# Performance work log

Hardware: AMD Instinct MI355X
Metric: run time of the kernel (lower is better)

## Reference

```python
import jax, jax.numpy as jnp
import numpy as np

B, TQ, TKV, NPR, H, D = 4, 1024, 1024, 5, 16, 64
IN, OUT, R, P, NT = 1024, H * D, 64, 4096, 4
KV = NPR + TKV  # prompt tokens prepended to kv sequence


def setup_inputs() -> dict:
    key = jax.random.key(0)
    ks = jax.random.split(key, 20)
    n = lambda k, shp, s: jax.random.normal(k, shp, jnp.float32) * s
    W = 0.02  # weight init scale
    return {
        "pe": n(ks[0], (P, OUT), 1.0),
        "attn_output": n(ks[1], (B, TQ, OUT), 1.0),
        "q": n(ks[2], (B, H, TQ, D), 1.0),
        "kv_query": n(ks[3], (B, TKV, IN), 1.0),
        "attn_mask": jnp.zeros((TQ, KV), jnp.float32),
        "prompt": n(ks[4], (NT, NPR, IN), 1.0),
        "gates": n(ks[5], (1,), 1.0),
        "k_w1": n(ks[6], (IN, R), W), "k_w2": n(ks[7], (R, OUT), W),
        "v_w1": n(ks[8], (IN, R), W), "v_w2": n(ks[9], (R, OUT), W),
        "kp_w1": n(ks[10], (OUT, R), W), "kp_w2": n(ks[11], (R, OUT), W),
        "qp_w1": n(ks[12], (OUT, R), W), "qp_w2": n(ks[13], (R, OUT), W),
        "indices_a": jax.random.randint(ks[14], (B, TQ), 0, P),
        "indices_b": jax.random.randint(ks[15], (B, TKV), 0, P),
        "task_idx": jax.random.randint(ks[16], (B,), 0, NT),
    }


def reference(pe, attn_output, q, kv_query, attn_mask, prompt, gates,
              k_w1, k_w2, v_w1, v_w2, kp_w1, kp_w2, qp_w1, qp_w2,
              indices_a, indices_b, task_idx):
    # prompt selection + concat in front of kv sequence
    pr = prompt[task_idx]                                   # [B, NPR, IN]
    kv_x = jnp.concatenate([pr, kv_query], axis=1)          # [B, KV, IN]
    # positional features; key_pos is zero-padded over the prompt slots
    key_pos = jnp.pad(pe[indices_b], ((0, 0), (NPR, 0), (0, 0)))  # [B, KV, OUT]
    # low-rank projections
    k = (kv_x @ k_w1) @ k_w2 + (key_pos @ kp_w1) @ kp_w2    # [B, KV, OUT]
    v = (kv_x @ v_w1) @ v_w2                                # [B, KV, OUT]
    q_pos = (pe[indices_a] @ qp_w1) @ qp_w2                 # [B, TQ, OUT]
    qh = q + q_pos.reshape(B, TQ, H, D).transpose(0, 2, 1, 3)
    kh = k.reshape(B, KV, H, D).transpose(0, 2, 1, 3)
    vh = v.reshape(B, KV, H, D).transpose(0, 2, 1, 3)
    scores = jnp.einsum('bhqd,bhkd->bhqk', qh, kh) / np.float32(np.sqrt(D))
    scores = scores + attn_mask[None, None]                 # 2D mask path
    w = jax.nn.softmax(scores, axis=-1)                     # dropout = identity (eval)
    out = jnp.einsum('bhqk,bhkd->bhqd', w, vh)
    out = out.transpose(0, 2, 1, 3).reshape(B, TQ, OUT)
    return out * gates + attn_output
```

## Files before the change

### kernel.cpp

```cpp
#include <hip/hip_runtime.h>
#include <hip/hip_bf16.h>

#define B_    4
#define TQ_   1024
#define TKV_  1024
#define NPR_  5
#define H_    16
#define D_    64
#define IN_   1024
#define OUT_  1024
#define R_    64
#define KV_   1029
#define KVP_  1088
#define M1_   4116
#define M1P_  4160
#define MQ_   4096
#define NKT_  17
#define NQT_  16
#define MR_   (M1P_ * R_)
#define LOG2E_ 1.4426950408889634f
#define SQ_SCALE_ (0.125f * 1.4426950408889634f)

typedef __attribute__((ext_vector_type(8))) short short8;
typedef __attribute__((ext_vector_type(4))) float f32x4;
typedef __attribute__((ext_vector_type(4))) unsigned uint4v;
typedef __attribute__((ext_vector_type(2))) unsigned uint2v;

#define MFMA(a, b, c) __builtin_amdgcn_mfma_f32_16x16x32_bf16(a, b, c, 0, 0, 0)

#define AS1 __attribute__((address_space(1)))
#define AS3 __attribute__((address_space(3)))
#define GLDS(g, l) __builtin_amdgcn_global_load_lds((const AS1 void*)(g), (AS3 void*)(l), 16, 0, 0)

static __device__ __forceinline__ short f2bf(float f) {
  unsigned u = __builtin_bit_cast(unsigned, f);
  u += 0x7fffu + ((u >> 16) & 1u);
  return (short)(u >> 16);
}
static __device__ __forceinline__ float bf2f(unsigned short u) {
  return __builtin_bit_cast(float, (unsigned)u << 16);
}
static __device__ __forceinline__ short8 zero8() {
  short8 z = {0, 0, 0, 0, 0, 0, 0, 0};
  return z;
}
static __device__ __forceinline__ unsigned cvtpk(float lo, float hi) {
  unsigned r;
  asm("v_cvt_pk_bf16_f32 %0, %1, %2" : "=v"(r) : "v"(lo), "v"(hi));
  return r;
}
static __device__ __forceinline__ float vexp2(float x) {
  float r;
  asm("v_exp_f32 %0, %1" : "=v"(r) : "v"(x));
  return r;
}
static __device__ __forceinline__ void pl32(unsigned &a, unsigned &b) {
  asm("v_permlane32_swap_b32 %0, %1" : "+v"(a), "+v"(b));
}
static __device__ __forceinline__ void pl16(unsigned &a, unsigned &b) {
  asm("v_permlane16_swap_b32 %0, %1" : "+v"(a), "+v"(b));
}
static __device__ __forceinline__ float redsum4(float x) {
  unsigned a = __builtin_bit_cast(unsigned, x), b = a;
  pl16(a, b);
  x = __builtin_bit_cast(float, a) + __builtin_bit_cast(float, b);
  a = b = __builtin_bit_cast(unsigned, x);
  pl32(a, b);
  return __builtin_bit_cast(float, a) + __builtin_bit_cast(float, b);
}
static __device__ __forceinline__ void cd2bfrag(const f32x4 (&s)[4], short8 &p0, short8 &p1) {
  unsigned u00 = cvtpk(s[0][0], s[0][1]), u01 = cvtpk(s[0][2], s[0][3]);
  unsigned u10 = cvtpk(s[1][0], s[1][1]), u11 = cvtpk(s[1][2], s[1][3]);
  unsigned u20 = cvtpk(s[2][0], s[2][1]), u21 = cvtpk(s[2][2], s[2][3]);
  unsigned u30 = cvtpk(s[3][0], s[3][1]), u31 = cvtpk(s[3][2], s[3][3]);
  pl32(u00, u10); pl32(u01, u11); pl32(u20, u30); pl32(u21, u31);
  pl16(u00, u10); pl16(u01, u11); pl16(u20, u30); pl16(u21, u31);
  uint4v w0 = {u00, u01, u10, u11};
  uint4v w1 = {u20, u21, u30, u31};
  p0 = __builtin_bit_cast(short8, w0);
  p1 = __builtin_bit_cast(short8, w1);
}
static __device__ __forceinline__ short8 sum4pack(const unsigned short* p) {
  f32x4 lo = {0, 0, 0, 0}, hi = {0, 0, 0, 0};
#pragma unroll
  for (int c = 0; c < 4; ++c) {
    short8 v = *(const short8*)(p + (size_t)c * MR_);
#pragma unroll
    for (int j = 0; j < 4; ++j) {
      lo[j] += bf2f((unsigned short)v[j]);
      hi[j] += bf2f((unsigned short)v[j + 4]);
    }
  }
  uint4v u = {cvtpk(lo[0], lo[1]), cvtpk(lo[2], lo[3]),
              cvtpk(hi[0], hi[1]), cvtpk(hi[2], hi[3])};
  return __builtin_bit_cast(short8, u);
}

__global__ __launch_bounds__(256) void prep(
    const float* __restrict__ kw1, const float* __restrict__ vw1,
    const float* __restrict__ kpw1, const float* __restrict__ qpw1,
    const float* __restrict__ kw2, const float* __restrict__ vw2,
    const float* __restrict__ kpw2, const float* __restrict__ qpw2,
    const float* __restrict__ mask, const float* __restrict__ pe,
    short* __restrict__ w1t, short* __restrict__ w2t,
    short* __restrict__ pebf, int* __restrict__ mflags) {
  int bid = blockIdx.x;
  if (bid < 64) {
    int tid = bid * 256 + threadIdx.x;
    const float* w1s[4] = {kw1, vw1, kpw1, qpw1};
    const float* w2s[4] = {kw2, vw2, kpw2, qpw2};
    for (int i = tid; i < 4 * R_ * IN_; i += 64 * 256) {
      int m = i >> 16, p = i & 65535, r = p >> 10, k = p & 1023;
      w1t[i] = f2bf(w1s[m][k * R_ + r]);
    }
    for (int i = tid; i < 4 * OUT_ * R_; i += 64 * 256) {
      int m = i >> 16, p = i & 65535, o = p >> 6, r = p & 63;
      w2t[i] = f2bf(w2s[m][r * OUT_ + o]);
    }
  } else if (bid < 336) {
    int t = bid - 64;
    int qt = t / NKT_, kt = t % NKT_;
    int nz = 0;
    for (int it = 0; it < 16; ++it) {
      int e = it * 256 + threadIdx.x;
      int rr = e >> 6, cc = e & 63;
      int kv = kt * 64 + cc;
      if (kv < KV_) {
        float v = mask[(size_t)(qt * 64 + rr) * KV_ + kv];
        nz |= (v != 0.0f);
      }
    }
    __shared__ int snz[4];
    unsigned long long bv = __ballot(nz);
    if ((threadIdx.x & 63) == 0) snz[threadIdx.x >> 6] = (bv != 0ULL);
    __syncthreads();
    if (threadIdx.x == 0) mflags[t] = snz[0] | snz[1] | snz[2] | snz[3];
  } else {
    int pb = bid - 336;
#pragma unroll
    for (int it = 0; it < 8; ++it) {
      int i = pb * 16384 + it * 2048 + threadIdx.x * 8;
      f32x4 a0 = *(const f32x4*)(pe + i);
      f32x4 a1 = *(const f32x4*)(pe + i + 4);
      uint4v u = {cvtpk(a0[0], a0[1]), cvtpk(a0[2], a0[3]),
                  cvtpk(a1[0], a1[1]), cvtpk(a1[2], a1[3])};
      *(uint4v*)(pebf + i) = u;
    }
  }
}

__global__ __launch_bounds__(256) void stage1(
    const float* __restrict__ prompt, const float* __restrict__ kv_query,
    const short* __restrict__ pebf, const int* __restrict__ indices_a,
    const int* __restrict__ indices_b, const int* __restrict__ task_idx,
    const short* __restrict__ w1t, unsigned short* __restrict__ part) {
  int which = blockIdx.z;
  int chunk = blockIdx.y;
  int mbase = blockIdx.x * 64;
  int lane = threadIdx.x & 63, wave = threadIdx.x >> 6;
  int lrow = lane & 15, lg = lane >> 4;
  int row = mbase + wave * 16 + lrow;

  const float* asrc_f = nullptr;
  const short* asrc_b = nullptr;
  if (which == 0) {
    int r = min(row, M1_ - 1);
    int b = r / KV_, t = r - b * KV_;
    asrc_f = (t < NPR_) ? prompt + (size_t)(task_idx[b] * NPR_ + t) * IN_
                        : kv_query + (size_t)(b * TKV_ + t - NPR_) * IN_;
  } else if (which == 1) {
    int r = min(row, M1_ - 1);
    int b = r / KV_, t = r - b * KV_;
    if (t >= NPR_) asrc_b = pebf + (size_t)indices_b[b * TKV_ + t - NPR_] * OUT_;
  } else {
    int r = min(row, MQ_ - 1);
    asrc_b = pebf + (size_t)indices_a[r] * OUT_;
  }
  const short* bt0 = w1t + (size_t)((which == 0) ? 0 : (which == 1) ? 2 : 3) * (R_ * IN_);
  const short* bt1 = w1t + (size_t)1 * (R_ * IN_);
  int k0base = chunk * 256;

  const f32x4 fz = {0, 0, 0, 0};
  f32x4 acc0[4], acc1[4];
#pragma unroll
  for (int f = 0; f < 4; ++f) { acc0[f] = fz; acc1[f] = fz; }

#pragma unroll
  for (int ks = 0; ks < 8; ++ks) {
    int kc = k0base + ks * 32 + lg * 8;
    short8 bdat;
    if (which == 0) {
      f32x4 a0 = *(const f32x4*)(asrc_f + kc);
      f32x4 a1 = *(const f32x4*)(asrc_f + kc + 4);
      uint4v au = {cvtpk(a0[0], a0[1]), cvtpk(a0[2], a0[3]),
                   cvtpk(a1[0], a1[1]), cvtpk(a1[2], a1[3])};
      bdat = __builtin_bit_cast(short8, au);
    } else {
      bdat = asrc_b ? *(const short8*)(asrc_b + kc) : zero8();
    }
#pragma unroll
    for (int f = 0; f < 4; ++f) {
      short8 w0 = *(const short8*)(bt0 + (size_t)(f * 16 + lrow) * IN_ + kc);
      acc0[f] = MFMA(w0, bdat, acc0[f]);
      if (which == 0) {
        short8 w1f = *(const short8*)(bt1 + (size_t)(f * 16 + lrow) * IN_ + kc);
        acc1[f] = MFMA(w1f, bdat, acc1[f]);
      }
    }
  }
  int o0 = (which == 0) ? 0 : (which == 1) ? 2 : 3;
  size_t mrow = (size_t)(mbase + wave * 16 + lrow) * R_;
  unsigned short* p0 = part + (size_t)(o0 * 4 + chunk) * MR_ + mrow;
#pragma unroll
  for (int f = 0; f < 4; ++f) {
    uint2v w = {cvtpk(acc0[f][0], acc0[f][1]), cvtpk(acc0[f][2], acc0[f][3])};
    *(uint2v*)(p0 + f * 16 + lg * 4) = w;
  }
  if (which == 0) {
    unsigned short* p1 = part + (size_t)(4 + chunk) * MR_ + mrow;
#pragma unroll
    for (int f = 0; f < 4; ++f) {
      uint2v w = {cvtpk(acc1[f][0], acc1[f][1]), cvtpk(acc1[f][2], acc1[f][3])};
      *(uint2v*)(p1 + f * 16 + lg * 4) = w;
    }
  }
}

__global__ __launch_bounds__(256) void stage2(
    const unsigned short* __restrict__ part, const short* __restrict__ w2t,
    short* __restrict__ kbf, short* __restrict__ vtb, short* __restrict__ tqs) {
  int L = blockIdx.x;
  int lane = threadIdx.x & 63, wave = threadIdx.x >> 6;
  int lrow = lane & 15, lg = lane >> 4;
  const f32x4 fz = {0, 0, 0, 0};

  if (L < 272) {
    int virt = (L & 7) * 34 + (L >> 3);
    int mt = virt >> 2, nh = virt & 3;
    int orow = mt * 64 + wave * 16 + lrow;
    int ob = orow / KVP_, okv = orow - ob * KVP_;
    bool valid = (okv < KV_);
    int kt = okv >> 6, rin = okv & 63;
    int prow = ob * KV_ + min(okv, KV_ - 1);
    short8 b1[2], b2[2];
#pragma unroll
    for (int ks = 0; ks < 2; ++ks) {
      int kc = ks * 32 + lg * 8;
      b1[ks] = valid ? sum4pack(part + (size_t)prow * R_ + kc) : zero8();
      b2[ks] = valid ? sum4pack(part + (size_t)8 * MR_ + (size_t)prow * R_ + kc) : zero8();
    }
    const short* w2k  = w2t;
    const short* w2kp = w2t + (size_t)2 * (OUT_ * R_);
    int sw = (rin & 7) << 3;
#pragma unroll
    for (int i = 0; i < 4; ++i) {
      int nbase = (nh * 4 + i) * 64;
      int h = nbase >> 6;
      f32x4 acc[4];
#pragma unroll
      for (int f = 0; f < 4; ++f) acc[f] = fz;
#pragma unroll
      for (int ks = 0; ks < 2; ++ks) {
        int kc = ks * 32 + lg * 8;
#pragma unroll
        for (int f = 0; f < 4; ++f) {
          short8 aK  = *(const short8*)(w2k  + (size_t)(nbase + f * 16 + lrow) * R_ + kc);
          short8 aKP = *(const short8*)(w2kp + (size_t)(nbase + f * 16 + lrow) * R_ + kc);
          acc[f] = MFMA(aK,  b1[ks], acc[f]);
          acc[f] = MFMA(aKP, b2[ks], acc[f]);
        }
      }
      size_t tb = ((size_t)((ob * H_ + h) * NKT_ + kt) << 12);
#pragma unroll
      for (int f = 0; f < 4; ++f) {
        float v0 = valid ? acc[f][0] : 0.f, v1 = valid ? acc[f][1] : 0.f;
        float v2 = valid ? acc[f][2] : 0.f, v3 = valid ? acc[f][3] : 0.f;
        uint2v w = {cvtpk(v0, v1), cvtpk(v2, v3)};
        int d0 = f * 16 + lg * 4;
        *(uint2v*)(kbf + tb + rin * 64 + (d0 ^ sw)) = w;
      }
    }
  } else if (L < 544) {
    int Lm = L - 272;
    int virt = (Lm & 7) * 34 + (Lm >> 3);
    int cb = virt >> 2, oh = virt & 3;
    short8 afr[8];
#pragma unroll
    for (int f = 0; f < 4; ++f)
#pragma unroll
      for (int ks = 0; ks < 2; ++ks) {
        int crow = cb * 64 + f * 16 + lrow;
        int bb = crow / KVP_, kvr = crow - bb * KVP_;
        afr[f * 2 + ks] = (kvr < KV_)
            ? sum4pack(part + (size_t)4 * MR_ + (size_t)(bb * KV_ + kvr) * R_ + ks * 32 + lg * 8)
            : zero8();
      }
    int bb = (cb * 64) / KVP_;
    int kvbase = cb * 64 - bb * KVP_;
    int kt = kvbase >> 6;
    const short* w2v = w2t + (size_t)1 * (OUT_ * R_);
#pragma unroll
    for (int i = 0; i < 4; ++i) {
      int obase = (oh * 4 + i) * 64;
      int o = obase + wave * 16 + lrow;
      int h = o >> 6, d = o & 63;
      f32x4 acc[4];
#pragma unroll
      for (int f = 0; f < 4; ++f) acc[f] = fz;
#pragma unroll
      for (int ks = 0; ks < 2; ++ks) {
        short8 bw = *(const short8*)(w2v + (size_t)o * R_ + ks * 32 + lg * 8);
#pragma unroll
        for (int f = 0; f < 4; ++f) acc[f] = MFMA(afr[f * 2 + ks], bw, acc[f]);
      }
      int sw = (d & 7) << 3;
      size_t tb = ((size_t)((bb * H_ + h) * NKT_ + kt) << 12);
#pragma unroll
      for (int f = 0; f < 4; ++f) {
        int kvin0 = f * 16 + lg * 4;
        float v0 = (kvbase + kvin0 + 0 < KV_) ? acc[f][0] : 0.f;
        float v1 = (kvbase + kvin0 + 1 < KV_) ? acc[f][1] : 0.f;
        float v2 = (kvbase + kvin0 + 2 < KV_) ? acc[f][2] : 0.f;
        float v3 = (kvbase + kvin0 + 3 < KV_) ? acc[f][3] : 0.f;
        uint2v w = {cvtpk(v0, v1), cvtpk(v2, v3)};
        *(uint2v*)(vtb + tb + d * 64 + (kvin0 ^ sw)) = w;
      }
    }
  } else {
    int j = L - 544;
#pragma unroll
    for (int it = 0; it < 8; ++it) {
      int idx = j * 16384 + it * 2048 + threadIdx.x * 8;
      short8 v = sum4pack(part + (size_t)12 * MR_ + idx);
      *(short8*)(tqs + idx) = v;
    }
  }
}

__global__ __launch_bounds__(256, 3) void attn(
    const short* __restrict__ tqs, const short* __restrict__ w2t,
    const float* __restrict__ qin,
    const short* __restrict__ kbf, const short* __restrict__ vtb,
    const float* __restrict__ mask, const int* __restrict__ mflags,
    const float* __restrict__ gates, const float* __restrict__ attn_in,
    float* __restrict__ out) {
  int bid = blockIdx.x;
  int xcd = bid & 7, rest = bid >> 3;
  int qsup = rest & 7, gi = rest >> 3;
  int grp = xcd * 8 + gi;
  int h = grp & 15, b = grp >> 4;

  int lane = threadIdx.x & 63, wave = threadIdx.x >> 6;
  int lrow = lane & 15, lg = lane >> 4;
  int qb = qsup * 128 + wave * 32;
  int qt = qsup * 2 + (wave >> 1);

  __shared__ __align__(16) short kvls[3][2][4096];

  const short* ktile = kbf + ((size_t)grp * NKT_ << 12);
  const short* vtile = vtb + ((size_t)grp * NKT_ << 12);
  const short* kg = ktile + wave * 512 + lane * 8;
  const short* vg = vtile + wave * 512 + lane * 8;

  int sw = (lrow & 7) << 3;
  int offA = (lg * 8) ^ sw;
  int offB = (32 + lg * 8) ^ sw;
  const short* p0A = &kvls[0][0][lrow * 64 + offA];
  const short* p0B = &kvls[0][0][lrow * 64 + offB];
  const short* p1A = &kvls[1][0][lrow * 64 + offA];
  const short* p1B = &kvls[1][0][lrow * 64 + offB];
  const short* p2A = &kvls[2][0][lrow * 64 + offA];
  const short* p2B = &kvls[2][0][lrow * 64 + offB];
  const int* mfp = mflags + qt * NKT_;

  auto stage = [&](int t, int bsel) {
    const short* ks = kg + ((size_t)t << 12);
    const short* vs = vg + ((size_t)t << 12);
    GLDS(ks,        &kvls[bsel][0][wave * 512]);
    GLDS(ks + 2048, &kvls[bsel][0][wave * 512 + 2048]);
    GLDS(vs,        &kvls[bsel][1][wave * 512]);
    GLDS(vs + 2048, &kvls[bsel][1][wave * 512 + 2048]);
  };

  stage(0, 0);
  stage(1, 1);

  int fl = 0;
#pragma unroll
  for (int t = 0; t < NKT_; ++t) fl |= (mfp[t] ? 1 : 0) << t;
  fl = __builtin_amdgcn_readfirstlane(fl);

  const f32x4 fz = {0, 0, 0, 0};
  short8 qa0[2], qa1[2];
#pragma unroll
  for (int p = 0; p < 2; ++p) {
    const short* w2q = w2t + (size_t)3 * (OUT_ * R_);
    f32x4 qs[4];
#pragma unroll
    for (int f = 0; f < 4; ++f) qs[f] = fz;
#pragma unroll
    for (int ks = 0; ks < 2; ++ks) {
      short8 tqf = *(const short8*)(tqs + (size_t)(b * TQ_ + qb + p * 16 + lrow) * R_ + ks * 32 + lg * 8);
#pragma unroll
      for (int f = 0; f < 4; ++f) {
        short8 wf = *(const short8*)(w2q + (size_t)(h * 64 + f * 16 + lrow) * R_ + ks * 32 + lg * 8);
        qs[f] = MFMA(wf, tqf, qs[f]);
      }
    }
    const float* qrow = qin + (size_t)(b * TQ_ + qb + p * 16 + lrow) * OUT_ + h * 64;
#pragma unroll
    for (int f = 0; f < 4; ++f) {
      f32x4 qv = *(const f32x4*)(qrow + f * 16 + lg * 4);
#pragma unroll
      for (int r = 0; r < 4; ++r) qs[f][r] = (qs[f][r] + qv[r]) * SQ_SCALE_;
    }
    cd2bfrag(qs, qa0[p], qa1[p]);
  }

  f32x4 oa0[4], oa1[4];
#pragma unroll
  for (int f = 0; f < 4; ++f) { oa0[f] = fz; oa1[f] = fz; }
  float plsum0 = 0.f, plsum1 = 0.f;

  auto tile = [&](int t, const short* pA, const short* pB, int sb, int mode) {
    if (mode == 2) asm volatile("s_waitcnt vmcnt(0)" ::: "memory");
    else           asm volatile("s_waitcnt vmcnt(4)" ::: "memory");
    __builtin_amdgcn_sched_barrier(0);
    __builtin_amdgcn_s_barrier();
    __builtin_amdgcn_sched_barrier(0);
    if (mode == 0) stage(t + 2, sb);

    f32x4 s0[4], s1[4];
#pragma unroll
    for (int f = 0; f < 4; ++f) {
      short8 kA = *(const short8*)(pA + f * 1024);
      short8 kB = *(const short8*)(pB + f * 1024);
      s0[f] = MFMA(kA, qa0[0], fz);
      s0[f] = MFMA(kB, qa1[0], s0[f]);
      s1[f] = MFMA(kA, qa0[1], fz);
      s1[f] = MFMA(kB, qa1[1], s1[f]);
    }
    if ((fl >> t) & 1) {
      int kvb = t * 64;
      const float* mrp0 = mask + (size_t)(qb + lrow) * KV_;
      const float* mrp1 = mask + (size_t)(qb + 16 + lrow) * KV_;
#pragma unroll
      for (int f = 0; f < 4; ++f)
#pragma unroll
        for (int r = 0; r < 4; ++r) {
          int kv = kvb + f * 16 + lg * 4 + r;
          if (kv < KV_) {
            s0[f][r] += mrp0[kv] * LOG2E_;
            s1[f][r] += mrp1[kv] * LOG2E_;
          }
        }
    }
    if (mode == 2) {
#pragma unroll
      for (int f = 0; f < 4; ++f)
#pragma unroll
        for (int r = 0; r < 4; ++r) {
          int kv = t * 64 + f * 16 + lg * 4 + r;
          if (kv >= KV_) { s0[f][r] = -1e30f; s1[f][r] = -1e30f; }
        }
    }
#pragma unroll
    for (int f = 0; f < 4; ++f)
#pragma unroll
      for (int r = 0; r < 4; ++r) {
        s0[f][r] = vexp2(s0[f][r]);
        s1[f][r] = vexp2(s1[f][r]);
      }
    f32x4 st0 = (s0[0] + s0[1]) + (s0[2] + s0[3]);
    f32x4 st1 = (s1[0] + s1[1]) + (s1[2] + s1[3]);
    plsum0 += (st0[0] + st0[1]) + (st0[2] + st0[3]);
    plsum1 += (st1[0] + st1[1]) + (st1[2] + st1[3]);
    short8 pbA0, pbA1, pbB0, pbB1;
    cd2bfrag(s0, pbA0, pbA1);
    cd2bfrag(s1, pbB0, pbB1);
#pragma unroll
    for (int f = 0; f < 4; ++f) {
      short8 vA = *(const short8*)(pA + 4096 + f * 1024);
      short8 vB = *(const short8*)(pB + 4096 + f * 1024);
      oa0[f] = MFMA(vA, pbA0, oa0[f]);
      oa0[f] = MFMA(vB, pbA1, oa0[f]);
      oa1[f] = MFMA(vA, pbB0, oa1[f]);
      oa1[f] = MFMA(vB, pbB1, oa1[f]);
    }
  };

#pragma unroll 1
  for (int i = 0; i < 5; ++i) {
    tile(3 * i + 0, p0A, p0B, 2, 0);
    tile(3 * i + 1, p1A, p1B, 0, 0);
    tile(3 * i + 2, p2A, p2B, 1, 0);
  }
  tile(15, p0A, p0B, 2, 1);
  tile(16, p1A, p1B, 0, 2);

  float lsum0 = redsum4(plsum0);
  float lsum1 = redsum4(plsum1);
  float g = gates[0];
  float sc0 = g / lsum0, sc1 = g / lsum1;
#pragma unroll
  for (int p = 0; p < 2; ++p) {
    float sc = p ? sc1 : sc0;
    const f32x4* oa = p ? oa1 : oa0;
    const float* ain = attn_in + (size_t)(b * TQ_ + qb + p * 16 + lrow) * OUT_ + h * 64;
    float* op = out + (size_t)(b * TQ_ + qb + p * 16 + lrow) * OUT_ + h * 64;
#pragma unroll
    for (int f = 0; f < 4; ++f) {
      f32x4 av = *(const f32x4*)(ain + f * 16 + lg * 4);
      f32x4 ov;
#pragma unroll
      for (int r = 0; r < 4; ++r) ov[r] = oa[f][r] * sc + av[r];
      *(f32x4*)(op + f * 16 + lg * 4) = ov;
    }
  }
}

extern "C" void kernel_launch(void* const* d_in, const int* in_sizes, int n_in,
                              void* d_out, int out_size, void* d_ws, size_t ws_size,
                              hipStream_t stream) {
  const float* pe          = (const float*)d_in[0];
  const float* attn_output = (const float*)d_in[1];
  const float* q           = (const float*)d_in[2];
  const float* kv_query    = (const float*)d_in[3];
  const float* attn_mask   = (const float*)d_in[4];
  const float* prompt      = (const float*)d_in[5];
  const float* gates       = (const float*)d_in[6];
  const float* k_w1        = (const float*)d_in[7];
  const float* k_w2        = (const float*)d_in[8];
  const float* v_w1        = (const float*)d_in[9];
  const float* v_w2        = (const float*)d_in[10];
  const float* kp_w1       = (const float*)d_in[11];
  const float* kp_w2       = (const float*)d_in[12];
  const float* qp_w1       = (const float*)d_in[13];
  const float* qp_w2       = (const float*)d_in[14];
  const int* indices_a     = (const int*)d_in[15];
  const int* indices_b     = (const int*)d_in[16];
  const int* task_idx      = (const int*)d_in[17];
  float* out = (float*)d_out;

  const size_t TILEB = (size_t)64 * NKT_ * 4096;

  short* ws   = (short*)d_ws;
  short* w1t  = ws;
  short* w2t  = w1t + 4 * 65536;
  unsigned short* part = (unsigned short*)(w2t + 4 * 65536);
  short* tqs  = (short*)(part + (size_t)16 * MR_);
  int* mflags = (int*)(tqs + (size_t)MQ_ * R_);
  short* pebf = (short*)mflags + 1024;
  short* kbf  = pebf;
  short* vtb  = kbf + TILEB;

  hipLaunchKernelGGL(prep, dim3(592), dim3(256), 0, stream,
                     k_w1, v_w1, kp_w1, qp_w1, k_w2, v_w2, kp_w2, qp_w2,
                     attn_mask, pe, w1t, w2t, pebf, mflags);
  hipLaunchKernelGGL(stage1, dim3(65, 4, 3), dim3(256), 0, stream,
                     prompt, kv_query, pebf, indices_a, indices_b, task_idx, w1t, part);
  hipLaunchKernelGGL(stage2, dim3(560), dim3(256), 0, stream,
                     part, w2t, kbf, vtb, tqs);
  hipLaunchKernelGGL(attn, dim3(512), dim3(256), 0, stream,
                     tqs, w2t, q, kbf, vtb, attn_mask, mflags, gates, attn_output, out);
}
```

Baseline: 109.3 us.

## Remap stage2 work so each block handles one (batch, head) across KV tiles

Stage2 is re-partitioned so each block owns one batch-head pair and loops over a strided set of KV tiles, computing all 64 output columns of that head. Blocks are grouped by XCD so a head's K and V tiles are produced on the same XCD, where the attention kernel presumably reads them. Before, each block computed one row tile for four heads. The grid shrinks from 560 to 528 blocks. The change aims to improve L2 locality of the written K/V tiles and of the w2 weight rows, at the cost of uneven work: sub 0 handles five tiles while the others handle four, and the per-block loop is serial.

```diff
diff --git a/kernel.cpp b/kernel.cpp
--- a/kernel.cpp
+++ b/kernel.cpp
@@ -229,105 +229,101 @@
 __global__ __launch_bounds__(256) void stage2(
     const unsigned short* __restrict__ part, const short* __restrict__ w2t,
     short* __restrict__ kbf, short* __restrict__ vtb, short* __restrict__ tqs) {
-  int L = blockIdx.x;
+  int bid = blockIdx.x;
   int lane = threadIdx.x & 63, wave = threadIdx.x >> 6;
   int lrow = lane & 15, lg = lane >> 4;
   const f32x4 fz = {0, 0, 0, 0};
 
-  if (L < 272) {
-    int virt = (L & 7) * 34 + (L >> 3);
-    int mt = virt >> 2, nh = virt & 3;
-    int orow = mt * 64 + wave * 16 + lrow;
-    int ob = orow / KVP_, okv = orow - ob * KVP_;
-    bool valid = (okv < KV_);
-    int kt = okv >> 6, rin = okv & 63;
-    int prow = ob * KV_ + min(okv, KV_ - 1);
-    short8 b1[2], b2[2];
-#pragma unroll
-    for (int ks = 0; ks < 2; ++ks) {
-      int kc = ks * 32 + lg * 8;
-      b1[ks] = valid ? sum4pack(part + (size_t)prow * R_ + kc) : zero8();
-      b2[ks] = valid ? sum4pack(part + (size_t)8 * MR_ + (size_t)prow * R_ + kc) : zero8();
-    }
-    const short* w2k  = w2t;
-    const short* w2kp = w2t + (size_t)2 * (OUT_ * R_);
-    int sw = (rin & 7) << 3;
-#pragma unroll
-    for (int i = 0; i < 4; ++i) {
-      int nbase = (nh * 4 + i) * 64;
-      int h = nbase >> 6;
-      f32x4 acc[4];
-#pragma unroll
-      for (int f = 0; f < 4; ++f) acc[f] = fz;
-#pragma unroll
-      for (int ks = 0; ks < 2; ++ks) {
-        int kc = ks * 32 + lg * 8;
+  if (bid < 512) {
+    int xcd = bid & 7, g2 = (bid >> 3) & 7, sub = bid >> 6;
+    int grp = xcd * 8 + g2;
+    int ob = grp >> 4, h = grp & 15;
+    if (sub < 4) {
+      const short* w2k  = w2t;
+      const short* w2kp = w2t + (size_t)2 * (OUT_ * R_);
+      int nk = (sub == 0) ? 5 : 4;
+      for (int j = 0; j < nk; ++j) {
+        int kt = (j == 4) ? 16 : sub + 4 * j;
+        int rin = wave * 16 + lrow;
+        int kv = kt * 64 + rin;
+        bool valid = (kv < KV_);
+        int prow = ob * KV_ + min(kv, KV_ - 1);
+        short8 b1[2], b2[2];
+#pragma unroll
+        for (int ks = 0; ks < 2; ++ks) {
+          int kc = ks * 32 + lg * 8;
+          b1[ks] = valid ? sum4pack(part + (size_t)prow * R_ + kc) : zero8();
+          b2[ks] = valid ? sum4pack(part + (size_t)8 * MR_ + (size_t)prow * R_ + kc) : zero8();
+        }
+        f32x4 acc[4];
+#pragma unroll
+        for (int f = 0; f < 4; ++f) acc[f] = fz;
+#pragma unroll
+        for (int ks = 0; ks < 2; ++ks) {
+          int kc = ks * 32 + lg * 8;
+#pragma unroll
+          for (int f = 0; f < 4; ++f) {
+            short8 aK  = *(const short8*)(w2k  + (size_t)(h * 64 + f * 16 + lrow) * R_ + kc);
+            short8 aKP = *(const short8*)(w2kp + (size_t)(h * 64 + f * 16 + lrow) * R_ + kc);
+            acc[f] = MFMA(aK,  b1[ks], acc[f]);
+            acc[f] = MFMA(aKP, b2[ks], acc[f]);
+          }
+        }
+        int sw = (rin & 7) << 3;
+        size_t tb = ((size_t)(grp * NKT_ + kt) << 12);
 #pragma unroll
         for (int f = 0; f < 4; ++f) {
-          short8 aK  = *(const short8*)(w2k  + (size_t)(nbase + f * 16 + lrow) * R_ + kc);
-          short8 aKP = *(const short8*)(w2kp + (size_t)(nbase + f * 16 + lrow) * R_ + kc);
-          acc[f] = MFMA(aK,  b1[ks], acc[f]);
-          acc[f] = MFMA(aKP, b2[ks], acc[f]);
+          float v0 = valid ? acc[f][0] : 0.f, v1 = valid ? acc[f][1] : 0.f;
+          float v2 = valid ? acc[f][2] : 0.f, v3 = valid ? acc[f][3] : 0.f;
+          uint2v w = {cvtpk(v0, v1), cvtpk(v2, v3)};
+          int d0 = f * 16 + lg * 4;
+          *(uint2v*)(kbf + tb + rin * 64 + (d0 ^ sw)) = w;
         }
       }
-      size_t tb = ((size_t)((ob * H_ + h) * NKT_ + kt) << 12);
-#pragma unroll
-      for (int f = 0; f < 4; ++f) {
-        float v0 = valid ? acc[f][0] : 0.f, v1 = valid ? acc[f][1] : 0.f;
-        float v2 = valid ? acc[f][2] : 0.f, v3 = valid ? acc[f][3] : 0.f;
-        uint2v w = {cvtpk(v0, v1), cvtpk(v2, v3)};
-        int d0 = f * 16 + lg * 4;
-        *(uint2v*)(kbf + tb + rin * 64 + (d0 ^ sw)) = w;
+    } else {
+      int s = sub - 4;
+      const short* w2v = w2t + (size_t)1 * (OUT_ * R_);
+      int nk = (s == 0) ? 5 : 4;
+      for (int j = 0; j < nk; ++j) {
+        int kt = (j == 4) ? 16 : s + 4 * j;
+        short8 afr[8];
+#pragma unroll
+        for (int f = 0; f < 4; ++f)
+#pragma unroll
+          for (int ks = 0; ks < 2; ++ks) {
+            int kvr = kt * 64 + f * 16 + lrow;
+            afr[f * 2 + ks] = (kvr < KV_)
+                ? sum4pack(part + (size_t)4 * MR_ + (size_t)(ob * KV_ + kvr) * R_ + ks * 32 + lg * 8)
+                : zero8();
+          }
+        int o = h * 64 + wave * 16 + lrow;
+        int d = wave * 16 + lrow;
+        f32x4 acc[4];
+#pragma unroll
+        for (int f = 0; f < 4; ++f) acc[f] = fz;
+#pragma unroll
+        for (int ks = 0; ks < 2; ++ks) {
+          short8 bw = *(const short8*)(w2v + (size_t)o * R_ + ks * 32 + lg * 8);
+#pragma unroll
+          for (int f = 0; f < 4; ++f) acc[f] = MFMA(afr[f * 2 + ks], bw, acc[f]);
+        }
+        int sw = (d & 7) << 3;
+        size_t tb = ((size_t)(grp * NKT_ + kt) << 12);
+        int kvbase = kt * 64;
+#pragma unroll
+        for (int f = 0; f < 4; ++f) {
+          int kvin0 = f * 16 + lg * 4;
+          float v0 = (kvbase + kvin0 + 0 < KV_) ? acc[f][0] : 0.f;
+          float v1 = (kvbase + kvin0 + 1 < KV_) ? acc[f][1] : 0.f;
+          float v2 = (kvbase + kvin0 + 2 < KV_) ? acc[f][2] : 0.f;
+          float v3 = (kvbase + kvin0 + 3 < KV_) ? acc[f][3] : 0.f;
+          uint2v w = {cvtpk(v0, v1), cvtpk(v2, v3)};
+          *(uint2v*)(vtb + tb + d * 64 + (kvin0 ^ sw)) = w;
+        }
       }
     }
-  } else if (L < 544) {
-    int Lm = L - 272;
-    int virt = (Lm & 7) * 34 + (Lm >> 3);
-    int cb = virt >> 2, oh = virt & 3;
-    short8 afr[8];
-#pragma unroll
-    for (int f = 0; f < 4; ++f)
-#pragma unroll
-      for (int ks = 0; ks < 2; ++ks) {
-        int crow = cb * 64 + f * 16 + lrow;
-        int bb = crow / KVP_, kvr = crow - bb * KVP_;
-        afr[f * 2 + ks] = (kvr < KV_)
-            ? sum4pack(part + (size_t)4 * MR_ + (size_t)(bb * KV_ + kvr) * R_ + ks * 32 + lg * 8)
-            : zero8();
-      }
-    int bb = (cb * 64) / KVP_;
-    int kvbase = cb * 64 - bb * KVP_;
-    int kt = kvbase >> 6;
-    const short* w2v = w2t + (size_t)1 * (OUT_ * R_);
-#pragma unroll
-    for (int i = 0; i < 4; ++i) {
-      int obase = (oh * 4 + i) * 64;
-      int o = obase + wave * 16 + lrow;
-      int h = o >> 6, d = o & 63;
-      f32x4 acc[4];
-#pragma unroll
-      for (int f = 0; f < 4; ++f) acc[f] = fz;
-#pragma unroll
-      for (int ks = 0; ks < 2; ++ks) {
-        short8 bw = *(const short8*)(w2v + (size_t)o * R_ + ks * 32 + lg * 8);
-#pragma unroll
-        for (int f = 0; f < 4; ++f) acc[f] = MFMA(afr[f * 2 + ks], bw, acc[f]);
-      }
-      int sw = (d & 7) << 3;
-      size_t tb = ((size_t)((bb * H_ + h) * NKT_ + kt) << 12);
-#pragma unroll
-      for (int f = 0; f < 4; ++f) {
-        int kvin0 = f * 16 + lg * 4;
-        float v0 = (kvbase + kvin0 + 0 < KV_) ? acc[f][0] : 0.f;
-        float v1 = (kvbase + kvin0 + 1 < KV_) ? acc[f][1] : 0.f;
-        float v2 = (kvbase + kvin0 + 2 < KV_) ? acc[f][2] : 0.f;
-        float v3 = (kvbase + kvin0 + 3 < KV_) ? acc[f][3] : 0.f;
-        uint2v w = {cvtpk(v0, v1), cvtpk(v2, v3)};
-        *(uint2v*)(vtb + tb + d * 64 + (kvin0 ^ sw)) = w;
-      }
-    }
   } else {
-    int j = L - 544;
+    int j = bid - 512;
 #pragma unroll
     for (int it = 0; it < 8; ++it) {
       int idx = j * 16384 + it * 2048 + threadIdx.x * 8;
@@ -559,7 +555,7 @@
                      attn_mask, pe, w1t, w2t, pebf, mflags);
   hipLaunchKernelGGL(stage1, dim3(65, 4, 3), dim3(256), 0, stream,
                      prompt, kv_query, pebf, indices_a, indices_b, task_idx, w1t, part);
-  hipLaunchKernelGGL(stage2, dim3(560), dim3(256), 0, stream,
+  hipLaunchKernelGGL(stage2, dim3(528), dim3(256), 0, stream,
                      part, w2t, kbf, vtb, tqs);
   hipLaunchKernelGGL(attn, dim3(512), dim3(256), 0, stream,
                      tqs, w2t, q, kbf, vtb, attn_mask, mflags, gates, attn_output, out);
```

Measured after the change: 120.7 us. 1.1x slower.
